# Performance work log

Hardware: AMD Instinct MI355X
Metric: run time of the kernel (lower is better)

## Reference

```python
import jax, jax.numpy as jnp
import numpy as np

B, T, D, H = 4, 2048, 1024, 16
HD = D // H  # head_dim = 64

def setup_inputs() -> dict:
    key = jax.random.key(0)
    k1, k2, k3 = jax.random.split(key, 3)
    s = 1.0 / np.sqrt(D)
    return {
        "x": jax.random.normal(k1, (B, T, D), dtype=jnp.float32),
        "w_qkv": jax.random.normal(k2, (D, 3 * D), dtype=jnp.float32) * s,
        "b_qkv": jnp.zeros((3 * D,), dtype=jnp.float32),
        "w_proj": jax.random.normal(k3, (D, D), dtype=jnp.float32) * s,
        "b_proj": jnp.zeros((D,), dtype=jnp.float32),
    }

def reference(x, w_qkv, b_qkv, w_proj, b_proj):
    b, t, c = x.shape
    qkv = x @ w_qkv + b_qkv                       # [B,T,3D]
    qkv = qkv.reshape(b, t, 3, H, HD)
    q, k, v = (jnp.transpose(qkv[:, :, i], (0, 2, 1, 3)) for i in range(3))  # [B,H,T,HD]
    scale = 1.0 / np.sqrt(HD)
    attn = jnp.einsum('bhqd,bhkd->bhqk', q, k) * scale  # [B,H,T,T]
    attn = jax.nn.softmax(attn, axis=-1)
    out = jnp.einsum('bhqk,bhkd->bhqd', attn, v)        # [B,H,T,HD]
    out = jnp.transpose(out, (0, 2, 1, 3)).reshape(b, t, c)
    return out @ w_proj + b_proj
```

## Files before the change

kernel.cpp:

```cpp
#include <hip/hip_runtime.h>
#include <hip/hip_bf16.h>

#define T_SEQ   2048
#define D_MODEL 1024
#define N_HEADS 16
#define HEAD_DIM 64
#define BT      8192
#define N3D     3072

using short8  = __attribute__((ext_vector_type(8))) short;
using short4v = __attribute__((ext_vector_type(4))) short;
using floatx4 = __attribute__((ext_vector_type(4))) float;

#define QSCALE 0.18033688f

__device__ __forceinline__ unsigned short rne_bf16(float f) {
  unsigned int u = __float_as_uint(f);
  u = (u + 0x7fffu + ((u >> 16) & 1u)) >> 16;
  return (unsigned short)u;
}

__device__ __forceinline__ void gload_lds16(const unsigned short* g,
                                            unsigned short* l) {
  __builtin_amdgcn_global_load_lds(
      (const __attribute__((address_space(1))) void*)g,
      (__attribute__((address_space(3))) void*)l, 16, 0, 0);
}

__global__ __launch_bounds__(256) void k_convert(const float* __restrict__ in,
                                                 unsigned short* __restrict__ out) {
  size_t i = ((size_t)blockIdx.x * 256 + threadIdx.x) * 8;
  float4 a = *(const float4*)(in + i);
  float4 b = *(const float4*)(in + i + 4);
  short8 v;
  v[0] = (short)rne_bf16(a.x); v[1] = (short)rne_bf16(a.y);
  v[2] = (short)rne_bf16(a.z); v[3] = (short)rne_bf16(a.w);
  v[4] = (short)rne_bf16(b.x); v[5] = (short)rne_bf16(b.y);
  v[6] = (short)rne_bf16(b.z); v[7] = (short)rne_bf16(b.w);
  *(short8*)(((short*)out) + i) = v;
}

__global__ __launch_bounds__(256) void k_transpose_convert(
    const float* __restrict__ in, unsigned short* __restrict__ out_hi,
    int R, int C) {
  __shared__ float tile[64][65];
  int tiles_c = C >> 6;
  int r0 = (blockIdx.x / tiles_c) << 6;
  int c0 = (blockIdx.x % tiles_c) << 6;
  int tid = threadIdx.x;
#pragma unroll
  for (int i = 0; i < 16; ++i) {
    int idx = tid + i * 256;
    int r = idx >> 6, c = idx & 63;
    tile[r][c] = in[(size_t)(r0 + r) * C + c0 + c];
  }
  __syncthreads();
#pragma unroll
  for (int i = 0; i < 16; ++i) {
    int idx = tid + i * 256;
    int orow = idx >> 6, oc = idx & 63;
    out_hi[(size_t)(c0 + orow) * R + r0 + oc] = rne_bf16(tile[oc][orow]);
  }
}

__global__ __launch_bounds__(256) void k_qkv_gemm(
    const unsigned short* __restrict__ A, const unsigned short* __restrict__ Bt,
    const float* __restrict__ bias,
    unsigned short* __restrict__ Qo, unsigned short* __restrict__ Ko,
    unsigned short* __restrict__ Vt) {
  __shared__ __align__(16) unsigned short As[128 * 32];
  __shared__ __align__(16) unsigned short Bs[128 * 32];
  int tid = threadIdx.x;
  int m0 = (blockIdx.x / 24) * 128;
  int n0 = (blockIdx.x % 24) * 128;
  int w = tid >> 6, lane = tid & 63, quad = lane >> 4, l16 = lane & 15;
  int wm = (w >> 1) * 64, wn = (w & 1) * 64;
  floatx4 acc[4][4] = {};

  int s_row[2], s_sp[2];
#pragma unroll
  for (int i = 0; i < 2; ++i) {
    int u = tid + i * 256;
    s_row[i] = u >> 2;
    s_sp[i] = (u & 3) ^ ((s_row[i] >> 1) & 3);
  }
  int a_off[4], b_off[4];
#pragma unroll
  for (int t = 0; t < 4; ++t) {
    int ra = wm + t * 16 + l16, rb = wn + t * 16 + l16;
    a_off[t] = ra * 32 + (quad ^ ((ra >> 1) & 3)) * 8;
    b_off[t] = rb * 32 + (quad ^ ((rb >> 1) & 3)) * 8;
  }

  for (int k0 = 0; k0 < 1024; k0 += 32) {
#pragma unroll
    for (int i = 0; i < 2; ++i) {
      int ub = (tid & ~63) + i * 256;
      gload_lds16(A + (size_t)(m0 + s_row[i]) * 1024 + k0 + s_sp[i] * 8,
                  &As[ub * 8]);
      gload_lds16(Bt + (size_t)(n0 + s_row[i]) * 1024 + k0 + s_sp[i] * 8,
                  &Bs[ub * 8]);
    }
    __syncthreads();
    short8 af[4], bf[4];
#pragma unroll
    for (int mt = 0; mt < 4; ++mt) af[mt] = *(const short8*)(&As[a_off[mt]]);
#pragma unroll
    for (int nt = 0; nt < 4; ++nt) bf[nt] = *(const short8*)(&Bs[b_off[nt]]);
#pragma unroll
    for (int mt = 0; mt < 4; ++mt)
#pragma unroll
      for (int nt = 0; nt < 4; ++nt)
        acc[mt][nt] = __builtin_amdgcn_mfma_f32_16x16x32_bf16(af[mt], bf[nt],
                                                              acc[mt][nt], 0, 0, 0);
    __syncthreads();
  }

#pragma unroll
  for (int nt = 0; nt < 4; ++nt) {
    int n = n0 + wn + nt * 16 + l16;
    float bv = bias[n];
    int which = n >> 10;
    int nn = n & 1023;
    int h = nn >> 6, hd = nn & 63;
#pragma unroll
    for (int mt = 0; mt < 4; ++mt) {
      int mbase = m0 + wm + mt * 16 + quad * 4;
      int b = mbase >> 11;
      int t0 = mbase & 2047;
      int head = b * N_HEADS + h;
      if (which == 2) {
        short4v vv;
#pragma unroll
        for (int r = 0; r < 4; ++r) vv[r] = (short)rne_bf16(acc[mt][nt][r] + bv);
        *(short4v*)(&Vt[((size_t)head * HEAD_DIM + hd) * T_SEQ + t0]) = vv;
      } else {
        unsigned short* dst = (which == 0) ? Qo : Ko;
        float scl = (which == 0) ? QSCALE : 1.0f;
#pragma unroll
        for (int r = 0; r < 4; ++r)
          dst[((size_t)head * T_SEQ + t0 + r) * HEAD_DIM + hd] =
              rne_bf16((acc[mt][nt][r] + bv) * scl);
      }
    }
  }
}

__global__ __launch_bounds__(256) void k_attn(
    const unsigned short* __restrict__ Q, const unsigned short* __restrict__ K,
    const unsigned short* __restrict__ Vt, unsigned short* __restrict__ Oo) {
  __shared__ __align__(16) unsigned short Klds[2][64 * 64];
  __shared__ __align__(16) unsigned short Vlds[2][64 * 64];
  int tid = threadIdx.x;
  int head = blockIdx.x >> 4;
  int qb = (blockIdx.x & 15) << 7;
  int b = head >> 4, h = head & 15;
  int w = tid >> 6, lane = tid & 63, quad = lane >> 4, l16 = lane & 15;
  const unsigned short* Qh = Q + (size_t)head * T_SEQ * HEAD_DIM;
  const unsigned short* Kh = K + (size_t)head * T_SEQ * HEAD_DIM;
  const unsigned short* Vh = Vt + (size_t)head * HEAD_DIM * T_SEQ;

  short8 qf[2][2];
#pragma unroll
  for (int qi = 0; qi < 2; ++qi) {
    int qrow = qb + w * 32 + qi * 16 + l16;
#pragma unroll
    for (int ks = 0; ks < 2; ++ks)
      qf[qi][ks] = *(const short8*)(Qh + (size_t)qrow * 64 + ks * 32 + quad * 8);
  }

  short8 ones;
#pragma unroll
  for (int j = 0; j < 8; ++j) ones[j] = (short)0x3F80;

  floatx4 O[2][4] = {};
  floatx4 Osum[2] = {};
  const floatx4 zf = {};

  int sg[2], sub[2], ksrc[2], vsrc[2];
#pragma unroll
  for (int i = 0; i < 2; ++i) {
    sg[i] = (tid + i * 256) >> 6;
    sub[i] = (tid & ~63) + i * 256;
    int xs = lane ^ sg[i];
    int ntp = xs >> 4, mp = xs & 15;
    ksrc[i] = ((ntp >> 1) << 5) + ((mp >> 2) << 3) + ((ntp & 1) << 2) + (mp & 3);
    vsrc[i] = xs;
  }

  int pu[2][4];
#pragma unroll
  for (int ks = 0; ks < 2; ++ks) {
    int gk = ks * 4 + quad;
#pragma unroll
    for (int t = 0; t < 4; ++t)
      pu[ks][t] = (((gk << 6) + t * 16 + l16) ^ gk) << 3;
  }

  auto stage = [&](int buf, int kb) {
#pragma unroll
    for (int i = 0; i < 2; ++i) {
      gload_lds16(Kh + ((size_t)(kb * 64 + ksrc[i])) * 64 + sg[i] * 8,
                  &Klds[buf][sub[i] * 8]);
      gload_lds16(Vh + (size_t)vsrc[i] * T_SEQ + kb * 64 + sg[i] * 8,
                  &Vlds[buf][sub[i] * 8]);
    }
  };

  auto compute = [&](const unsigned short* Kb_, const unsigned short* Vb_) {
    floatx4 s[2][4];
    __builtin_amdgcn_s_setprio(1);
#pragma unroll
    for (int ks = 0; ks < 2; ++ks) {
#pragma unroll
      for (int nt = 0; nt < 4; ++nt) {
        short8 kf = *(const short8*)(Kb_ + pu[ks][nt]);
        if (ks == 0) {
          s[0][nt] = __builtin_amdgcn_mfma_f32_16x16x32_bf16(kf, qf[0][0], zf, 0, 0, 0);
          s[1][nt] = __builtin_amdgcn_mfma_f32_16x16x32_bf16(kf, qf[1][0], zf, 0, 0, 0);
        } else {
          s[0][nt] = __builtin_amdgcn_mfma_f32_16x16x32_bf16(kf, qf[0][1], s[0][nt], 0, 0, 0);
          s[1][nt] = __builtin_amdgcn_mfma_f32_16x16x32_bf16(kf, qf[1][1], s[1][nt], 0, 0, 0);
        }
      }
    }
    __builtin_amdgcn_s_setprio(0);

    short8 pB[2][2];
#pragma unroll
    for (int qi = 0; qi < 2; ++qi) {
      unsigned int dw[4][2];
#pragma unroll
      for (int nt = 0; nt < 4; ++nt) {
        float p0 = __builtin_amdgcn_exp2f(s[qi][nt][0]);
        float p1 = __builtin_amdgcn_exp2f(s[qi][nt][1]);
        float p2 = __builtin_amdgcn_exp2f(s[qi][nt][2]);
        float p3 = __builtin_amdgcn_exp2f(s[qi][nt][3]);
        __hip_bfloat162 lo2 = __float22bfloat162_rn(make_float2(p0, p1));
        __hip_bfloat162 hi2 = __float22bfloat162_rn(make_float2(p2, p3));
        dw[nt][0] = *(unsigned int*)&lo2;
        dw[nt][1] = *(unsigned int*)&hi2;
      }
#pragma unroll
      for (int ks = 0; ks < 2; ++ks) {
        union { unsigned int u[4]; short8 s8; } cv;
        cv.u[0] = dw[2 * ks][0];
        cv.u[1] = dw[2 * ks][1];
        cv.u[2] = dw[2 * ks + 1][0];
        cv.u[3] = dw[2 * ks + 1][1];
        pB[qi][ks] = cv.s8;
      }
    }

#pragma unroll
    for (int ks = 0; ks < 2; ++ks) {
      __builtin_amdgcn_s_setprio(1);
      Osum[0] = __builtin_amdgcn_mfma_f32_16x16x32_bf16(ones, pB[0][ks], Osum[0], 0, 0, 0);
      Osum[1] = __builtin_amdgcn_mfma_f32_16x16x32_bf16(ones, pB[1][ks], Osum[1], 0, 0, 0);
#pragma unroll
      for (int dt = 0; dt < 4; ++dt) {
        short8 vf = *(const short8*)(Vb_ + pu[ks][dt]);
        O[0][dt] = __builtin_amdgcn_mfma_f32_16x16x32_bf16(vf, pB[0][ks], O[0][dt], 0, 0, 0);
        O[1][dt] = __builtin_amdgcn_mfma_f32_16x16x32_bf16(vf, pB[1][ks], O[1][dt], 0, 0, 0);
      }
      __builtin_amdgcn_s_setprio(0);
    }
  };

  stage(0, 0);
  __syncthreads();

#pragma unroll 1
  for (int kb = 0; kb < 32; kb += 2) {
    stage(1, kb + 1);
    compute(&Klds[0][0], &Vlds[0][0]);
    __syncthreads();
    if (kb + 2 < 32) stage(0, kb + 2);
    compute(&Klds[1][0], &Vlds[1][0]);
    __syncthreads();
  }

#pragma unroll
  for (int qi = 0; qi < 2; ++qi) {
    float inv = 1.0f / Osum[qi][0];
    int t = qb + w * 32 + qi * 16 + l16;
    size_t rowo = ((size_t)(b * T_SEQ + t)) * D_MODEL + h * HEAD_DIM;
#pragma unroll
    for (int dt = 0; dt < 4; ++dt) {
      short4v ov;
#pragma unroll
      for (int r = 0; r < 4; ++r) ov[r] = (short)rne_bf16(O[qi][dt][r] * inv);
      *(short4v*)(&Oo[rowo + dt * 16 + quad * 4]) = ov;
    }
  }
}

__global__ __launch_bounds__(256) void k_proj_gemm(
    const unsigned short* __restrict__ A, const unsigned short* __restrict__ Bt,
    const float* __restrict__ bias, float* __restrict__ out) {
  __shared__ __align__(16) unsigned short As[128 * 32];
  __shared__ __align__(16) unsigned short Bs[128 * 32];
  int tid = threadIdx.x;
  int m0 = (blockIdx.x >> 3) * 128;
  int n0 = (blockIdx.x & 7) * 128;
  int w = tid >> 6, lane = tid & 63, quad = lane >> 4, l16 = lane & 15;
  int wm = (w >> 1) * 64, wn = (w & 1) * 64;
  floatx4 acc[4][4] = {};

  int s_row[2], s_sp[2];
#pragma unroll
  for (int i = 0; i < 2; ++i) {
    int u = tid + i * 256;
    s_row[i] = u >> 2;
    s_sp[i] = (u & 3) ^ ((s_row[i] >> 1) & 3);
  }
  int a_off[4], b_off[4];
#pragma unroll
  for (int t = 0; t < 4; ++t) {
    int ra = wm + t * 16 + l16, rb = wn + t * 16 + l16;
    a_off[t] = ra * 32 + (quad ^ ((ra >> 1) & 3)) * 8;
    b_off[t] = rb * 32 + (quad ^ ((rb >> 1) & 3)) * 8;
  }

  for (int k0 = 0; k0 < 1024; k0 += 32) {
#pragma unroll
    for (int i = 0; i < 2; ++i) {
      int ub = (tid & ~63) + i * 256;
      gload_lds16(A + (size_t)(m0 + s_row[i]) * 1024 + k0 + s_sp[i] * 8,
                  &As[ub * 8]);
      gload_lds16(Bt + (size_t)(n0 + s_row[i]) * 1024 + k0 + s_sp[i] * 8,
                  &Bs[ub * 8]);
    }
    __syncthreads();
    short8 af[4], bf[4];
#pragma unroll
    for (int mt = 0; mt < 4; ++mt) af[mt] = *(const short8*)(&As[a_off[mt]]);
#pragma unroll
    for (int nt = 0; nt < 4; ++nt) bf[nt] = *(const short8*)(&Bs[b_off[nt]]);
#pragma unroll
    for (int mt = 0; mt < 4; ++mt)
#pragma unroll
      for (int nt = 0; nt < 4; ++nt)
        acc[mt][nt] = __builtin_amdgcn_mfma_f32_16x16x32_bf16(af[mt], bf[nt],
                                                              acc[mt][nt], 0, 0, 0);
    __syncthreads();
  }

#pragma unroll
  for (int nt = 0; nt < 4; ++nt) {
    int n = n0 + wn + nt * 16 + l16;
    float bv = bias[n];
#pragma unroll
    for (int mt = 0; mt < 4; ++mt)
#pragma unroll
      for (int r = 0; r < 4; ++r) {
        int m = m0 + wm + mt * 16 + quad * 4 + r;
        out[(size_t)m * 1024 + n] = acc[mt][nt][r] + bv;
      }
  }
}

extern "C" void kernel_launch(void* const* d_in, const int* in_sizes, int n_in,
                              void* d_out, int out_size, void* d_ws, size_t ws_size,
                              hipStream_t stream) {
  const float* x     = (const float*)d_in[0];
  const float* wqkv  = (const float*)d_in[1];
  const float* bqkv  = (const float*)d_in[2];
  const float* wproj = (const float*)d_in[3];
  const float* bproj = (const float*)d_in[4];

  char* ws = (char*)d_ws;
  size_t off = 0;
  unsigned short* x_bf  = (unsigned short*)(ws + off); off += (size_t)BT * D_MODEL * 2;
  unsigned short* wq_T  = (unsigned short*)(ws + off); off += (size_t)N3D * D_MODEL * 2;
  unsigned short* wp_T  = (unsigned short*)(ws + off); off += (size_t)D_MODEL * D_MODEL * 2;
  unsigned short* Qb    = (unsigned short*)(ws + off); off += (size_t)BT * D_MODEL * 2;
  unsigned short* Kb    = (unsigned short*)(ws + off); off += (size_t)BT * D_MODEL * 2;
  unsigned short* Vt    = (unsigned short*)(ws + off); off += (size_t)BT * D_MODEL * 2;
  unsigned short* a_bf  = (unsigned short*)(ws + off); off += (size_t)BT * D_MODEL * 2;

  k_convert<<<(BT * D_MODEL) / (256 * 8), 256, 0, stream>>>(x, x_bf);
  k_transpose_convert<<<(1024 / 64) * (3072 / 64), 256, 0, stream>>>(wqkv, wq_T, 1024, 3072);
  k_transpose_convert<<<(1024 / 64) * (1024 / 64), 256, 0, stream>>>(wproj, wp_T, 1024, 1024);
  k_qkv_gemm<<<(BT / 128) * (N3D / 128), 256, 0, stream>>>(x_bf, wq_T, bqkv, Qb, Kb, Vt);
  k_attn<<<(T_SEQ / 128) * 4 * N_HEADS, 256, 0, stream>>>(Qb, Kb, Vt, a_bf);
  k_proj_gemm<<<(BT / 128) * (D_MODEL / 128), 256, 0, stream>>>(a_bf, wp_T, bproj, (float*)d_out);
}
```

Measured before the change: 310.8 us.

## Double-buffer GEMM K-loops and software-pipeline attention QK with previous PV

Both GEMM kernels now stage the next K-slice into a second LDS buffer while computing on the current one, removing the load-then-wait stall per iteration. The attention kernel is restructured so each iteration issues QK for block t together with PV for block t-1 (using a triple-buffered V in LDS), keeping the matrix units busy while the exponentials for the current block run afterwards. It also adds a launch-bounds occupancy hint of 4 blocks. This costs more LDS and registers, which could cut occupancy or cause spills.

```diff
diff --git a/kernel.cpp b/kernel.cpp
--- a/kernel.cpp
+++ b/kernel.cpp
@@ -68,8 +68,8 @@
     const float* __restrict__ bias,
     unsigned short* __restrict__ Qo, unsigned short* __restrict__ Ko,
     unsigned short* __restrict__ Vt) {
-  __shared__ __align__(16) unsigned short As[128 * 32];
-  __shared__ __align__(16) unsigned short Bs[128 * 32];
+  __shared__ __align__(16) unsigned short As[2][128 * 32];
+  __shared__ __align__(16) unsigned short Bs[2][128 * 32];
   int tid = threadIdx.x;
   int m0 = (blockIdx.x / 24) * 128;
   int n0 = (blockIdx.x % 24) * 128;
@@ -92,27 +92,39 @@
     b_off[t] = rb * 32 + (quad ^ ((rb >> 1) & 3)) * 8;
   }
 
-  for (int k0 = 0; k0 < 1024; k0 += 32) {
+  auto stage = [&](int buf, int k0) {
 #pragma unroll
     for (int i = 0; i < 2; ++i) {
       int ub = (tid & ~63) + i * 256;
       gload_lds16(A + (size_t)(m0 + s_row[i]) * 1024 + k0 + s_sp[i] * 8,
-                  &As[ub * 8]);
+                  &As[buf][ub * 8]);
       gload_lds16(Bt + (size_t)(n0 + s_row[i]) * 1024 + k0 + s_sp[i] * 8,
-                  &Bs[ub * 8]);
-    }
+                  &Bs[buf][ub * 8]);
+    }
+  };
+  auto compute = [&](int buf) {
+    short8 af[4], bfr[4];
+#pragma unroll
+    for (int mt = 0; mt < 4; ++mt) af[mt] = *(const short8*)(&As[buf][a_off[mt]]);
+#pragma unroll
+    for (int nt = 0; nt < 4; ++nt) bfr[nt] = *(const short8*)(&Bs[buf][b_off[nt]]);
+#pragma unroll
+    for (int mt = 0; mt < 4; ++mt)
+#pragma unroll
+      for (int nt = 0; nt < 4; ++nt)
+        acc[mt][nt] = __builtin_amdgcn_mfma_f32_16x16x32_bf16(af[mt], bfr[nt],
+                                                              acc[mt][nt], 0, 0, 0);
+  };
+
+  stage(0, 0);
+  __syncthreads();
+#pragma unroll 1
+  for (int k0 = 0; k0 < 1024; k0 += 64) {
+    stage(1, k0 + 32);
+    compute(0);
     __syncthreads();
-    short8 af[4], bf[4];
-#pragma unroll
-    for (int mt = 0; mt < 4; ++mt) af[mt] = *(const short8*)(&As[a_off[mt]]);
-#pragma unroll
-    for (int nt = 0; nt < 4; ++nt) bf[nt] = *(const short8*)(&Bs[b_off[nt]]);
-#pragma unroll
-    for (int mt = 0; mt < 4; ++mt)
-#pragma unroll
-      for (int nt = 0; nt < 4; ++nt)
-        acc[mt][nt] = __builtin_amdgcn_mfma_f32_16x16x32_bf16(af[mt], bf[nt],
-                                                              acc[mt][nt], 0, 0, 0);
+    if (k0 + 64 < 1024) stage(0, k0 + 64);
+    compute(1);
     __syncthreads();
   }
 
@@ -146,11 +158,11 @@
   }
 }
 
-__global__ __launch_bounds__(256) void k_attn(
+__global__ __launch_bounds__(256, 4) void k_attn(
     const unsigned short* __restrict__ Q, const unsigned short* __restrict__ K,
     const unsigned short* __restrict__ Vt, unsigned short* __restrict__ Oo) {
   __shared__ __align__(16) unsigned short Klds[2][64 * 64];
-  __shared__ __align__(16) unsigned short Vlds[2][64 * 64];
+  __shared__ __align__(16) unsigned short Vlds[3][64 * 64];
   int tid = threadIdx.x;
   int head = blockIdx.x >> 4;
   int qb = (blockIdx.x & 15) << 7;
@@ -197,19 +209,22 @@
       pu[ks][t] = (((gk << 6) + t * 16 + l16) ^ gk) << 3;
   }
 
-  auto stage = [&](int buf, int kb) {
-#pragma unroll
-    for (int i = 0; i < 2; ++i) {
+  auto stageK = [&](unsigned short* dst, int kb) {
+#pragma unroll
+    for (int i = 0; i < 2; ++i)
       gload_lds16(Kh + ((size_t)(kb * 64 + ksrc[i])) * 64 + sg[i] * 8,
-                  &Klds[buf][sub[i] * 8]);
+                  dst + sub[i] * 8);
+  };
+  auto stageV = [&](unsigned short* dst, int kb) {
+#pragma unroll
+    for (int i = 0; i < 2; ++i)
       gload_lds16(Vh + (size_t)vsrc[i] * T_SEQ + kb * 64 + sg[i] * 8,
-                  &Vlds[buf][sub[i] * 8]);
-    }
-  };
-
-  auto compute = [&](const unsigned short* Kb_, const unsigned short* Vb_) {
-    floatx4 s[2][4];
-    __builtin_amdgcn_s_setprio(1);
+                  dst + sub[i] * 8);
+  };
+
+  short8 pPrev[2][2];
+
+  auto qk = [&](const unsigned short* Kb_, floatx4 (&s)[2][4]) {
 #pragma unroll
     for (int ks = 0; ks < 2; ++ks) {
 #pragma unroll
@@ -224,9 +239,23 @@
         }
       }
     }
-    __builtin_amdgcn_s_setprio(0);
-
-    short8 pB[2][2];
+  };
+
+  auto pv = [&](const unsigned short* Vb_) {
+#pragma unroll
+    for (int ks = 0; ks < 2; ++ks) {
+      Osum[0] = __builtin_amdgcn_mfma_f32_16x16x32_bf16(ones, pPrev[0][ks], Osum[0], 0, 0, 0);
+      Osum[1] = __builtin_amdgcn_mfma_f32_16x16x32_bf16(ones, pPrev[1][ks], Osum[1], 0, 0, 0);
+#pragma unroll
+      for (int dt = 0; dt < 4; ++dt) {
+        short8 vf = *(const short8*)(Vb_ + pu[ks][dt]);
+        O[0][dt] = __builtin_amdgcn_mfma_f32_16x16x32_bf16(vf, pPrev[0][ks], O[0][dt], 0, 0, 0);
+        O[1][dt] = __builtin_amdgcn_mfma_f32_16x16x32_bf16(vf, pPrev[1][ks], O[1][dt], 0, 0, 0);
+      }
+    }
+  };
+
+  auto expPack = [&](floatx4 (&s)[2][4]) {
 #pragma unroll
     for (int qi = 0; qi < 2; ++qi) {
       unsigned int dw[4][2];
@@ -248,37 +277,41 @@
         cv.u[1] = dw[2 * ks][1];
         cv.u[2] = dw[2 * ks + 1][0];
         cv.u[3] = dw[2 * ks + 1][1];
-        pB[qi][ks] = cv.s8;
-      }
-    }
-
-#pragma unroll
-    for (int ks = 0; ks < 2; ++ks) {
-      __builtin_amdgcn_s_setprio(1);
-      Osum[0] = __builtin_amdgcn_mfma_f32_16x16x32_bf16(ones, pB[0][ks], Osum[0], 0, 0, 0);
-      Osum[1] = __builtin_amdgcn_mfma_f32_16x16x32_bf16(ones, pB[1][ks], Osum[1], 0, 0, 0);
-#pragma unroll
-      for (int dt = 0; dt < 4; ++dt) {
-        short8 vf = *(const short8*)(Vb_ + pu[ks][dt]);
-        O[0][dt] = __builtin_amdgcn_mfma_f32_16x16x32_bf16(vf, pB[0][ks], O[0][dt], 0, 0, 0);
-        O[1][dt] = __builtin_amdgcn_mfma_f32_16x16x32_bf16(vf, pB[1][ks], O[1][dt], 0, 0, 0);
-      }
-      __builtin_amdgcn_s_setprio(0);
-    }
-  };
-
-  stage(0, 0);
+        pPrev[qi][ks] = cv.s8;
+      }
+    }
+  };
+
+  unsigned short* Kcur = &Klds[1][0];
+  unsigned short* Koth = &Klds[0][0];
+  unsigned short* Vp = &Vlds[0][0];
+  unsigned short* Vc = &Vlds[1][0];
+  unsigned short* Vn = &Vlds[2][0];
+
+  stageK(Koth, 0); stageV(Vp, 0);
   __syncthreads();
+  stageK(Kcur, 1); stageV(Vc, 1);
+  {
+    floatx4 s[2][4];
+    qk(Koth, s);
+    expPack(s);
+  }
+  __syncthreads();
 
 #pragma unroll 1
-  for (int kb = 0; kb < 32; kb += 2) {
-    stage(1, kb + 1);
-    compute(&Klds[0][0], &Vlds[0][0]);
+  for (int t = 1; t < 32; ++t) {
+    if (t < 31) { stageK(Koth, t + 1); stageV(Vn, t + 1); }
+    floatx4 s[2][4];
+    __builtin_amdgcn_s_setprio(1);
+    qk(Kcur, s);
+    pv(Vp);
+    __builtin_amdgcn_s_setprio(0);
+    expPack(s);
     __syncthreads();
-    if (kb + 2 < 32) stage(0, kb + 2);
-    compute(&Klds[1][0], &Vlds[1][0]);
-    __syncthreads();
-  }
+    unsigned short* tk = Kcur; Kcur = Koth; Koth = tk;
+    unsigned short* tv = Vp; Vp = Vc; Vc = Vn; Vn = tv;
+  }
+  pv(Vp);
 
 #pragma unroll
   for (int qi = 0; qi < 2; ++qi) {
@@ -298,8 +331,8 @@
 __global__ __launch_bounds__(256) void k_proj_gemm(
     const unsigned short* __restrict__ A, const unsigned short* __restrict__ Bt,
     const float* __restrict__ bias, float* __restrict__ out) {
-  __shared__ __align__(16) unsigned short As[128 * 32];
-  __shared__ __align__(16) unsigned short Bs[128 * 32];
+  __shared__ __align__(16) unsigned short As[2][128 * 32];
+  __shared__ __align__(16) unsigned short Bs[2][128 * 32];
   int tid = threadIdx.x;
   int m0 = (blockIdx.x >> 3) * 128;
   int n0 = (blockIdx.x & 7) * 128;
@@ -322,27 +355,39 @@
     b_off[t] = rb * 32 + (quad ^ ((rb >> 1) & 3)) * 8;
   }
 
-  for (int k0 = 0; k0 < 1024; k0 += 32) {
+  auto stage = [&](int buf, int k0) {
 #pragma unroll
     for (int i = 0; i < 2; ++i) {
       int ub = (tid & ~63) + i * 256;
       gload_lds16(A + (size_t)(m0 + s_row[i]) * 1024 + k0 + s_sp[i] * 8,
-                  &As[ub * 8]);
+                  &As[buf][ub * 8]);
       gload_lds16(Bt + (size_t)(n0 + s_row[i]) * 1024 + k0 + s_sp[i] * 8,
-                  &Bs[ub * 8]);
-    }
+                  &Bs[buf][ub * 8]);
+    }
+  };
+  auto compute = [&](int buf) {
+    short8 af[4], bfr[4];
+#pragma unroll
+    for (int mt = 0; mt < 4; ++mt) af[mt] = *(const short8*)(&As[buf][a_off[mt]]);
+#pragma unroll
+    for (int nt = 0; nt < 4; ++nt) bfr[nt] = *(const short8*)(&Bs[buf][b_off[nt]]);
+#pragma unroll
+    for (int mt = 0; mt < 4; ++mt)
+#pragma unroll
+      for (int nt = 0; nt < 4; ++nt)
+        acc[mt][nt] = __builtin_amdgcn_mfma_f32_16x16x32_bf16(af[mt], bfr[nt],
+                                                              acc[mt][nt], 0, 0, 0);
+  };
+
+  stage(0, 0);
+  __syncthreads();
+#pragma unroll 1
+  for (int k0 = 0; k0 < 1024; k0 += 64) {
+    stage(1, k0 + 32);
+    compute(0);
     __syncthreads();
-    short8 af[4], bf[4];
-#pragma unroll
-    for (int mt = 0; mt < 4; ++mt) af[mt] = *(const short8*)(&As[a_off[mt]]);
-#pragma unroll
-    for (int nt = 0; nt < 4; ++nt) bf[nt] = *(const short8*)(&Bs[b_off[nt]]);
-#pragma unroll
-    for (int mt = 0; mt < 4; ++mt)
-#pragma unroll
-      for (int nt = 0; nt < 4; ++nt)
-        acc[mt][nt] = __builtin_amdgcn_mfma_f32_16x16x32_bf16(af[mt], bf[nt],
-                                                              acc[mt][nt], 0, 0, 0);
+    if (k0 + 64 < 1024) stage(0, k0 + 64);
+    compute(1);
     __syncthreads();
   }
 
```

New measurement: 324.9 us. +4.5%, slower.

## Software-pipeline attention: overlap QK of next tile with PV of previous, 512-thread blocks

Applied to the files above, without the earlier changes.

Restructures the attention kernel so each iteration computes QK^T for the current key tile and PV for the previous tile's probabilities, with exp/pack after the MFMA burst, using triple-buffered V and double-buffered K in LDS. Blocks grow to 512 threads (8 waves, 256 query rows), which halves the grid and shares each K/V tile across twice as many queries. Block-to-head mapping is remapped to interleave heads across the grid. The goal is to hide exp latency behind matrix work and to cut global K/V traffic, at the cost of more LDS and registers per block, which may lower occupancy.

```diff
diff --git a/kernel.cpp b/kernel.cpp
--- a/kernel.cpp
+++ b/kernel.cpp
@@ -146,14 +146,14 @@
   }
 }
 
-__global__ __launch_bounds__(256) void k_attn(
+__global__ __launch_bounds__(512, 4) void k_attn(
     const unsigned short* __restrict__ Q, const unsigned short* __restrict__ K,
     const unsigned short* __restrict__ Vt, unsigned short* __restrict__ Oo) {
   __shared__ __align__(16) unsigned short Klds[2][64 * 64];
-  __shared__ __align__(16) unsigned short Vlds[2][64 * 64];
+  __shared__ __align__(16) unsigned short Vlds[3][64 * 64];
   int tid = threadIdx.x;
-  int head = blockIdx.x >> 4;
-  int qb = (blockIdx.x & 15) << 7;
+  int head = ((blockIdx.x & 7) << 3) + (blockIdx.x >> 6);
+  int qb = ((blockIdx.x >> 3) & 7) << 8;
   int b = head >> 4, h = head & 15;
   int w = tid >> 6, lane = tid & 63, quad = lane >> 4, l16 = lane & 15;
   const unsigned short* Qh = Q + (size_t)head * T_SEQ * HEAD_DIM;
@@ -177,16 +177,12 @@
   floatx4 Osum[2] = {};
   const floatx4 zf = {};
 
-  int sg[2], sub[2], ksrc[2], vsrc[2];
-#pragma unroll
-  for (int i = 0; i < 2; ++i) {
-    sg[i] = (tid + i * 256) >> 6;
-    sub[i] = (tid & ~63) + i * 256;
-    int xs = lane ^ sg[i];
-    int ntp = xs >> 4, mp = xs & 15;
-    ksrc[i] = ((ntp >> 1) << 5) + ((mp >> 2) << 3) + ((ntp & 1) << 2) + (mp & 3);
-    vsrc[i] = xs;
-  }
+  int sg = tid >> 6;
+  int xs = lane ^ sg;
+  int ntp = xs >> 4, mp = xs & 15;
+  int ksrc = ((ntp >> 1) << 5) + ((mp >> 2) << 3) + ((ntp & 1) << 2) + (mp & 3);
+  int vsrc = xs;
+  int sub = tid & ~63;
 
   int pu[2][4];
 #pragma unroll
@@ -197,19 +193,16 @@
       pu[ks][t] = (((gk << 6) + t * 16 + l16) ^ gk) << 3;
   }
 
-  auto stage = [&](int buf, int kb) {
-#pragma unroll
-    for (int i = 0; i < 2; ++i) {
-      gload_lds16(Kh + ((size_t)(kb * 64 + ksrc[i])) * 64 + sg[i] * 8,
-                  &Klds[buf][sub[i] * 8]);
-      gload_lds16(Vh + (size_t)vsrc[i] * T_SEQ + kb * 64 + sg[i] * 8,
-                  &Vlds[buf][sub[i] * 8]);
-    }
-  };
-
-  auto compute = [&](const unsigned short* Kb_, const unsigned short* Vb_) {
-    floatx4 s[2][4];
-    __builtin_amdgcn_s_setprio(1);
+  auto stageK = [&](unsigned short* dst, int kb) {
+    gload_lds16(Kh + ((size_t)(kb * 64 + ksrc)) * 64 + sg * 8, dst + sub * 8);
+  };
+  auto stageV = [&](unsigned short* dst, int kb) {
+    gload_lds16(Vh + (size_t)vsrc * T_SEQ + kb * 64 + sg * 8, dst + sub * 8);
+  };
+
+  short8 pPrev[2][2];
+
+  auto qk = [&](const unsigned short* Kb_, floatx4 (&s)[2][4]) {
 #pragma unroll
     for (int ks = 0; ks < 2; ++ks) {
 #pragma unroll
@@ -224,9 +217,23 @@
         }
       }
     }
-    __builtin_amdgcn_s_setprio(0);
-
-    short8 pB[2][2];
+  };
+
+  auto pv = [&](const unsigned short* Vb_) {
+#pragma unroll
+    for (int ks = 0; ks < 2; ++ks) {
+      Osum[0] = __builtin_amdgcn_mfma_f32_16x16x32_bf16(ones, pPrev[0][ks], Osum[0], 0, 0, 0);
+      Osum[1] = __builtin_amdgcn_mfma_f32_16x16x32_bf16(ones, pPrev[1][ks], Osum[1], 0, 0, 0);
+#pragma unroll
+      for (int dt = 0; dt < 4; ++dt) {
+        short8 vf = *(const short8*)(Vb_ + pu[ks][dt]);
+        O[0][dt] = __builtin_amdgcn_mfma_f32_16x16x32_bf16(vf, pPrev[0][ks], O[0][dt], 0, 0, 0);
+        O[1][dt] = __builtin_amdgcn_mfma_f32_16x16x32_bf16(vf, pPrev[1][ks], O[1][dt], 0, 0, 0);
+      }
+    }
+  };
+
+  auto expPack = [&](floatx4 (&s)[2][4]) {
 #pragma unroll
     for (int qi = 0; qi < 2; ++qi) {
       unsigned int dw[4][2];
@@ -248,37 +255,41 @@
         cv.u[1] = dw[2 * ks][1];
         cv.u[2] = dw[2 * ks + 1][0];
         cv.u[3] = dw[2 * ks + 1][1];
-        pB[qi][ks] = cv.s8;
-      }
-    }
-
-#pragma unroll
-    for (int ks = 0; ks < 2; ++ks) {
-      __builtin_amdgcn_s_setprio(1);
-      Osum[0] = __builtin_amdgcn_mfma_f32_16x16x32_bf16(ones, pB[0][ks], Osum[0], 0, 0, 0);
-      Osum[1] = __builtin_amdgcn_mfma_f32_16x16x32_bf16(ones, pB[1][ks], Osum[1], 0, 0, 0);
-#pragma unroll
-      for (int dt = 0; dt < 4; ++dt) {
-        short8 vf = *(const short8*)(Vb_ + pu[ks][dt]);
-        O[0][dt] = __builtin_amdgcn_mfma_f32_16x16x32_bf16(vf, pB[0][ks], O[0][dt], 0, 0, 0);
-        O[1][dt] = __builtin_amdgcn_mfma_f32_16x16x32_bf16(vf, pB[1][ks], O[1][dt], 0, 0, 0);
-      }
-      __builtin_amdgcn_s_setprio(0);
-    }
-  };
-
-  stage(0, 0);
+        pPrev[qi][ks] = cv.s8;
+      }
+    }
+  };
+
+  unsigned short* Kcur = &Klds[1][0];
+  unsigned short* Koth = &Klds[0][0];
+  unsigned short* Vp = &Vlds[0][0];
+  unsigned short* Vc = &Vlds[1][0];
+  unsigned short* Vn = &Vlds[2][0];
+
+  stageK(Koth, 0); stageV(Vp, 0);
   __syncthreads();
+  stageK(Kcur, 1); stageV(Vc, 1);
+  {
+    floatx4 s[2][4];
+    qk(Koth, s);
+    expPack(s);
+  }
+  __syncthreads();
 
 #pragma unroll 1
-  for (int kb = 0; kb < 32; kb += 2) {
-    stage(1, kb + 1);
-    compute(&Klds[0][0], &Vlds[0][0]);
-    __syncthreads();
-    if (kb + 2 < 32) stage(0, kb + 2);
-    compute(&Klds[1][0], &Vlds[1][0]);
-    __syncthreads();
-  }
+  for (int t = 1; t < 32; ++t) {
+    if (t < 31) { stageK(Koth, t + 1); stageV(Vn, t + 1); }
+    floatx4 s[2][4];
+    __builtin_amdgcn_s_setprio(1);
+    qk(Kcur, s);
+    pv(Vp);
+    __builtin_amdgcn_s_setprio(0);
+    expPack(s);
+    __syncthreads();
+    unsigned short* tk = Kcur; Kcur = Koth; Koth = tk;
+    unsigned short* tv = Vp; Vp = Vc; Vc = Vn; Vn = tv;
+  }
+  pv(Vp);
 
 #pragma unroll
   for (int qi = 0; qi < 2; ++qi) {
@@ -383,6 +394,6 @@
   k_transpose_convert<<<(1024 / 64) * (3072 / 64), 256, 0, stream>>>(wqkv, wq_T, 1024, 3072);
   k_transpose_convert<<<(1024 / 64) * (1024 / 64), 256, 0, stream>>>(wproj, wp_T, 1024, 1024);
   k_qkv_gemm<<<(BT / 128) * (N3D / 128), 256, 0, stream>>>(x_bf, wq_T, bqkv, Qb, Kb, Vt);
-  k_attn<<<(T_SEQ / 128) * 4 * N_HEADS, 256, 0, stream>>>(Qb, Kb, Vt, a_bf);
+  k_attn<<<512, 512, 0, stream>>>(Qb, Kb, Vt, a_bf);
   k_proj_gemm<<<(BT / 128) * (D_MODEL / 128), 256, 0, stream>>>(a_bf, wp_T, bproj, (float*)d_out);
 }
```

After: 282.6 us. 1.1x faster.
